# Optimization experiments

Measured on AMD Instinct MI355X. Metric: run time of the kernel, lower is better.

The kernel has to match this reference:

```python
import jax, jax.numpy as jnp
import numpy as np

D, H, B = 16, 1024, 2048  # input_size, hidden_size, batch
EPS = 1e-12


def _masks():
    # MADE degree assignment, order 'A' (natural order)
    deg_in = jnp.arange(1, D + 1)                # [D]
    deg_h = jnp.arange(H) % (D - 1) + 1          # [H]
    m0 = (deg_h[:, None] >= deg_in[None, :]).astype(jnp.float32)  # [H, D] input->hidden
    m1 = (deg_h[:, None] >= deg_h[None, :]).astype(jnp.float32)   # [H, H] hidden->hidden
    m2 = (deg_in[:, None] > deg_h[None, :]).astype(jnp.float32)   # [D, H] hidden->output
    return m0, m1, m2


def setup_inputs() -> dict:
    key = jax.random.key(0)
    ks = jax.random.split(key, 8)

    def lin(k, out_d, in_d):
        k1, k2, k3 = jax.random.split(k, 3)
        v = jax.random.normal(k1, (out_d, in_d), jnp.float32)
        g = jax.random.uniform(k2, (out_d,), jnp.float32, 0.1, 0.2)  # small gain keeps logstd stable over D iters
        b = jax.random.normal(k3, (out_d,), jnp.float32) * 0.01
        return v, g, b

    inp = {"x": jax.random.normal(ks[0], (B, D), jnp.float32)}
    dims = [(H, D), (H, H), (D, H)]
    i = 1
    for n in ("mu", "lv"):
        for j, (o, ii) in enumerate(dims):
            v, g, b = lin(ks[i], o, ii)
            i += 1
            inp[f"{n}_v{j}"] = v
            inp[f"{n}_g{j}"] = g
            inp[f"{n}_b{j}"] = b
    return inp


def _wn(v, g, m):
    # weight-normalized masked linear weight: mask * g * v / ||v||
    return m * (g[:, None] * v / jnp.linalg.norm(v, axis=1, keepdims=True))


def _made(y, p):
    (w0, b0), (w1, b1), (w2, b2) = p
    h = jax.nn.elu(y @ w0.T + b0)   # [B, H]
    h = jax.nn.elu(h @ w1.T + b1)   # [B, H]
    return h @ w2.T + b2            # [B, D]


def reference(x, mu_v0, mu_g0, mu_b0, mu_v1, mu_g1, mu_b1, mu_v2, mu_g2, mu_b2,
              lv_v0, lv_g0, lv_b0, lv_v1, lv_g1, lv_b1, lv_v2, lv_g2, lv_b2):
    m0, m1, m2 = _masks()
    pm = ((_wn(mu_v0, mu_g0, m0), mu_b0), (_wn(mu_v1, mu_g1, m1), mu_b1), (_wn(mu_v2, mu_g2, m2), mu_b2))
    pl = ((_wn(lv_v0, lv_g0, m0), lv_b0), (_wn(lv_v1, lv_g1, m1), lv_b1), (_wn(lv_v2, lv_g2, m2), lv_b2))

    def step(carry, _):
        y, _ls = carry
        mu = _made(y, pm)
        logstd = _made(y, pl) * 0.5
        y_new = (x - mu) / (jnp.exp(logstd) + EPS)
        return (y_new, logstd), None

    init = (jnp.zeros_like(x), jnp.zeros_like(x))
    (y, logstd), _ = jax.lax.scan(step, init, None, length=D)
    return y, logstd.sum(axis=1)
```

## Files before the change

kernel.cpp:

```cpp
#include <hip/hip_runtime.h>
#include <cstdint>
#include <cstddef>


#define Dd 16
#define Hh 1024
#define Bb 2048
#define EPSV 1e-12f

typedef unsigned short u16;
typedef __attribute__((ext_vector_type(4))) float f32x4;
typedef __attribute__((ext_vector_type(8))) short s16x8;
typedef __attribute__((ext_vector_type(4))) u16 u16x4;
typedef __attribute__((ext_vector_type(8))) u16 u16x8;

__device__ __forceinline__ u16 f2bf(float f) {
  union { float f; unsigned u; } v; v.f = f;
  unsigned u = v.u;
  unsigned r = (u + 0x7fffu + ((u >> 16) & 1u)) >> 16;
  return (u16)r;
}
__device__ __forceinline__ float elu(float a) {
  return a > 0.f ? a : __expf(a) - 1.f;
}
__device__ __forceinline__ void barrier_lds() {
  asm volatile("s_waitcnt lgkmcnt(0)" ::: "memory");
  __builtin_amdgcn_s_barrier();
}

__device__ __forceinline__ int p_of(int i) {
  if (i < 276) { int g = i / 69, q = i - g * 69; return g + 15 * q; }
  int r = i - 276; int g = 4 + r / 68, q = r - (g - 4) * 68;
  return g + 15 * q;
}
__device__ __forceinline__ int g_of(int i) {
  return (i < 276) ? (i / 69) : (4 + (i - 276) / 68);
}
__device__ __forceinline__ int lb_of(int g) {
  return (g <= 4) ? 69 * g : 276 + 68 * (g - 4);
}
__device__ __forceinline__ int sz_of(int g) { return (g < 4) ? 69 : 68; }

#define W2F_NET (15 * 3 * 512)
#define W0F_NET (15 * 5 * 512)

__global__ __launch_bounds__(256) void prep_all(
    const float* __restrict__ mu_v0, const float* __restrict__ mu_g0,
    const float* __restrict__ mu_b0,
    const float* __restrict__ mu_v1, const float* __restrict__ mu_g1,
    const float* __restrict__ mu_b1,
    const float* __restrict__ mu_v2, const float* __restrict__ mu_g2,
    const float* __restrict__ lv_v0, const float* __restrict__ lv_g0,
    const float* __restrict__ lv_b0,
    const float* __restrict__ lv_v1, const float* __restrict__ lv_g1,
    const float* __restrict__ lv_b1,
    const float* __restrict__ lv_v2, const float* __restrict__ lv_g2,
    u16* __restrict__ W1f, u16* __restrict__ W2f, u16* __restrict__ W0f,
    float* __restrict__ b1p, float* __restrict__ b0p) {
  int bid = blockIdx.x, tid = threadIdx.x;
  int l = tid & 63, w = tid >> 6;

  {
    int wid = bid * 4 + w;
    int net = wid / 1200, rem = wid % 1200;
    int g = rem / 80, u = rem % 80;
    u16* dstb = W1f + ((size_t)((net * 15 + g) * 16) * 10) * 512;
    const int nf = u >> 4, lane16 = u & 15;
    if (u < sz_of(g)) {
      int j = p_of(lb_of(g) + u);
      const float* v = (net ? lv_v1 : mu_v1) + (size_t)j * Hh;
      float val[4][4]; float ss = 0.f;
      for (int ii = 0; ii < 4; ++ii)
        for (int t = 0; t < 4; ++t) {
          int kp = ii * 256 + 4 * l + t;
          float xx = v[p_of(kp)];
          val[ii][t] = xx; ss += xx * xx;
        }
      for (int s = 32; s; s >>= 1) ss += __shfl_xor(ss, s);
      float sc = ((net ? lv_g1 : mu_g1)[j]) * rsqrtf(ss);
      for (int ii = 0; ii < 4; ++ii) {
        int k0 = ii * 256 + 4 * l;
        u16x4 wv;
        for (int t = 0; t < 4; ++t)
          wv[t] = f2bf((g >= g_of(k0 + t)) ? sc * val[ii][t] : 0.f);
        int kt = k0 >> 6, kk = (k0 >> 5) & 1;
        int lanep = lane16 + 16 * ((k0 & 31) >> 3);
        *(u16x4*)(dstb + (size_t)(kt * 10 + nf * 2 + kk) * 512 +
                  lanep * 8 + (k0 & 7)) = wv;
      }
      if (l == 0) b1p[wid] = (net ? lv_b1 : mu_b1)[j];
    } else {
      u16x4 z = {0, 0, 0, 0};
      for (int ii = 0; ii < 4; ++ii) {
        int k0 = ii * 256 + 4 * l;
        int kt = k0 >> 6, kk = (k0 >> 5) & 1;
        int lanep = lane16 + 16 * ((k0 & 31) >> 3);
        *(u16x4*)(dstb + (size_t)(kt * 10 + nf * 2 + kk) * 512 +
                  lanep * 8 + (k0 & 7)) = z;
      }
      if (l == 0) b1p[wid] = 0.f;
    }
  }

  if (bid < 8) {
    int wid2 = bid * 4 + w;
    int nn = wid2 >> 4, oi = wid2 & 15;
    const float* v = (nn ? lv_v2 : mu_v2) + (size_t)oi * Hh;
    float ss = 0.f;
    for (int ii = 0; ii < 4; ++ii) {
      f32x4 vv = *(const f32x4*)(v + ii * 256 + 4 * l);
      ss += vv[0]*vv[0] + vv[1]*vv[1] + vv[2]*vv[2] + vv[3]*vv[3];
    }
    for (int s = 32; s; s >>= 1) ss += __shfl_xor(ss, s);
    float sc = ((nn ? lv_g2 : mu_g2)[oi]) * rsqrtf(ss);
    for (int e = l; e < 180; e += 64) {
      int g = e / 12, r12 = e - g * 12;
      int c = r12 >> 2, lk2 = r12 & 3;
      u16x8 wv;
      for (int t = 0; t < 8; ++t) {
        int u = c * 32 + lk2 * 8 + t;
        float val = (u < sz_of(g) && oi > g) ? sc * v[p_of(lb_of(g) + u)]
                                             : 0.f;
        wv[t] = f2bf(val);
      }
      *(u16x8*)(W2f + (size_t)(nn * W2F_NET) + ((g * 3 + c) * 64 +
                (oi + 16 * lk2)) * 8) = wv;
    }
  }

  if (bid >= 8 && bid < 18) {
    int idx = (bid - 8) * 256 + tid;
    if (idx < 2400) {
      int nn = idx / 1200, rem = idx % 1200;
      int g = rem / 80, u = rem % 80;
      const int nf = u >> 4, lr16 = u & 15;
      float row[16];
      float bias = 0.f;
      if (u < sz_of(g)) {
        int j = p_of(lb_of(g) + u);
        const float* v = (nn ? lv_v0 : mu_v0) + j * Dd;
        float vv[16]; float ss = 0.f;
        for (int k = 0; k < 16; ++k) { vv[k] = v[k]; ss += vv[k] * vv[k]; }
        float sc = ((nn ? lv_g0 : mu_g0)[j]) * rsqrtf(ss);
        for (int k = 0; k < 16; ++k) row[k] = (g >= k) ? sc * vv[k] : 0.f;
        bias = (nn ? lv_b0 : mu_b0)[j];
      } else {
        for (int k = 0; k < 16; ++k) row[k] = 0.f;
      }
      for (int lk2 = 0; lk2 < 4; ++lk2) {
        u16x8 wv;
        for (int t = 0; t < 8; ++t) {
          int k = lk2 * 8 + t;
          wv[t] = f2bf((k < 16) ? row[k] : 0.f);
        }
        *(u16x8*)(W0f + (size_t)(nn * W0F_NET) + ((g * 5 + nf) * 64 +
                  (lr16 + 16 * lk2)) * 8) = wv;
      }
      b0p[nn * 1200 + g * 80 + u] = bias;
    }
  }
}

#define LOADF(DST, BASE, KT)                                                \
  {                                                                         \
    const u16* fp_ = (BASE) + (size_t)(KT) * 5120;                          \
    _Pragma("unroll") for (int nf_ = 0; nf_ < 5; ++nf_)                     \
      _Pragma("unroll") for (int kk_ = 0; kk_ < 2; ++kk_)                   \
        DST[nf_][kk_] = *(const s16x8*)(fp_ + (nf_ * 2 + kk_) * 512);       \
  }
#define MFMAI(SLOT, KT)                                                     \
  {                                                                         \
    s16x8 a0_ = *(const s16x8*)(&h0L[net][lr][(KT) * 64 + lk * 8]);         \
    s16x8 a1_ = *(const s16x8*)(&h0L[net][lr][(KT) * 64 + 32 + lk * 8]);    \
    _Pragma("unroll") for (int nf_ = 0; nf_ < 5; ++nf_) {                   \
      hacc[nf_] = __builtin_amdgcn_mfma_f32_16x16x32_bf16(                  \
          a0_, SLOT[nf_][0], hacc[nf_], 0, 0, 0);                           \
      hacc[nf_] = __builtin_amdgcn_mfma_f32_16x16x32_bf16(                  \
          a1_, SLOT[nf_][1], hacc[nf_], 0, 0, 0);                           \
    }                                                                       \
  }

__global__ __launch_bounds__(512, 1) void afmade_main(
    const u16* __restrict__ W1f, const u16* __restrict__ W2f,
    const u16* __restrict__ W0f,
    const float* __restrict__ b1p, const float* __restrict__ b0p,
    const float* __restrict__ b2_mu, const float* __restrict__ b2_lv,
    const float* __restrict__ x, float* __restrict__ out) {
  __shared__ u16 h0L[2][16][1040];
  __shared__ float sPart[2][4][16][80];
  __shared__ u16 sH1[2][16][104];
  __shared__ u16 yb[16][40];
  __shared__ float sX[16][16];
  __shared__ float sB1L[2400];
  __shared__ float sB0L[2400];
  __shared__ float sB2[2][16];
  __shared__ float sLsum[16];

  const int tid = threadIdx.x;
  const int l = tid & 63, w = tid >> 6;
  const int net = w >> 2, kq = w & 3;
  const int lr = l & 15, lk = l >> 4;
  const int b0g = blockIdx.x * 16;

  {
    u16x8 z = {0, 0, 0, 0, 0, 0, 0, 0};
    for (int e = tid; e < 4160; e += 512) ((u16x8*)h0L)[e] = z;
    for (int e = tid; e < 416; e += 512) ((u16x8*)sH1)[e] = z;
    for (int e = tid; e < 80; e += 512) ((u16x8*)yb)[e] = z;
  }
  for (int e = tid; e < 256; e += 512)
    sX[e >> 4][e & 15] = x[(size_t)(b0g + (e >> 4)) * 16 + (e & 15)];
  for (int e = tid; e < 2400; e += 512) { sB1L[e] = b1p[e]; sB0L[e] = b0p[e]; }
  if (tid < 16) sB2[0][tid] = b2_mu[tid];
  else if (tid < 32) sB2[1][tid - 16] = b2_lv[tid - 16];
  else if (tid < 48) sLsum[tid - 32] = 0.f;
  f32x4 mlacc0 = {0.f, 0.f, 0.f, 0.f};
  f32x4 mlacc1 = {0.f, 0.f, 0.f, 0.f};

  s16x8 bfA[5][2], bfB[5][2];
  {
    const u16* base1 = W1f + ((size_t)((net * 15 + 0) * 16) * 10) * 512 +
                       (size_t)l * 8;
    if (kq < 2) LOADF(bfA, base1, kq);
  }
  __syncthreads();

  for (int s = 0; s < 16; ++s) {
    s16x8 w0pre0, w0pre1;
    if (s < 15) {
      const u16* W0g = W0f + net * W0F_NET + s * (5 * 512);
      w0pre0 = *(const s16x8*)(W0g + (size_t)kq * 512 + l * 8);
      if (kq == 0)
        w0pre1 = *(const s16x8*)(W0g + (size_t)4 * 512 + l * 8);
    }

    if (s > 0) {
      const int g = s - 1;
      const int ktn = (lb_of(s) + 63) >> 6;
      const int ktnN = (s < 15) ? ((lb_of(s + 1) + 63) >> 6) : 0;
      const u16* baseg = W1f + ((size_t)((net * 15 + g) * 16) * 10) * 512 +
                         (size_t)l * 8;
      const u16* basen = W1f + ((size_t)((net * 15 + s) * 16) * 10) * 512 +
                         (size_t)l * 8;
      s16x8 w2f[6];
#pragma unroll
      for (int c = 0; c < 3; ++c) {
        w2f[c] = *(const s16x8*)(W2f + ((size_t)(g * 3 + c) * 64 + l) * 8);
        w2f[3 + c] = *(const s16x8*)(W2f + (size_t)W2F_NET +
                                     ((size_t)(g * 3 + c) * 64 + l) * 8);
      }
      f32x4 hacc[5] = {};
      if (kq + 4 < ktn)  LOADF(bfB, baseg, kq + 4);
      if (kq < ktn)      MFMAI(bfA, kq);
      if (kq + 8 < ktn)  LOADF(bfA, baseg, kq + 8);
      if (kq + 4 < ktn)  MFMAI(bfB, kq + 4);
      if (kq + 12 < ktn) LOADF(bfB, baseg, kq + 12);
      if (kq + 8 < ktn)  MFMAI(bfA, kq + 8);
      if (kq + 12 < ktn) MFMAI(bfB, kq + 12);
#pragma unroll
      for (int nf = 0; nf < 5; ++nf)
#pragma unroll
        for (int reg = 0; reg < 4; ++reg)
          sPart[net][kq][lk * 4 + reg][nf * 16 + lr] = hacc[nf][reg];
      if (s < 15 && kq < ktnN) LOADF(bfA, basen, kq);
      barrier_lds();
      {
        const int nn = tid >> 8;
        const int rr = (tid >> 4) & 15;
        const int u0 = tid & 15;
#pragma unroll
        for (int c = 0; c < 5; ++c) {
          int uu = c * 16 + u0;
          float v = sPart[nn][0][rr][uu] + sPart[nn][1][rr][uu] +
                    sPart[nn][2][rr][uu] + sPart[nn][3][rr][uu] +
                    sB1L[nn * 1200 + g * 80 + uu];
          sH1[nn][rr][uu] = f2bf(elu(v));
        }
      }
      barrier_lds();
#pragma unroll
      for (int c = 0; c < 3; ++c) {
        s16x8 a0 = *(const s16x8*)(&sH1[0][lr][c * 32 + lk * 8]);
        mlacc0 = __builtin_amdgcn_mfma_f32_16x16x32_bf16(
            a0, w2f[c], mlacc0, 0, 0, 0);
        s16x8 a1v = *(const s16x8*)(&sH1[1][lr][c * 32 + lk * 8]);
        mlacc1 = __builtin_amdgcn_mfma_f32_16x16x32_bf16(
            a1v, w2f[3 + c], mlacc1, 0, 0, 0);
      }
    }
    if (lr == s) {
#pragma unroll
      for (int reg = 0; reg < 4; ++reg) {
        int r = lk * 4 + reg;
        float mu = mlacc0[reg] + sB2[0][s];
        float lv = mlacc1[reg] + sB2[1][s];
        float ls = 0.5f * lv;
        float yv = (sX[r][s] - mu) / (__expf(ls) + EPSV);
        yb[r][s] = f2bf(yv);
        if (w == 0) {
          out[(size_t)(b0g + r) * 16 + s] = yv;
          float ns = sLsum[r] + ls;
          sLsum[r] = ns;
          if (s == 15) out[Bb * 16 + b0g + r] = ns;
        }
      }
    }
    asm volatile("s_waitcnt lgkmcnt(0)" ::: "memory");
    if (s < 15) {
      const int LbS = lb_of(s), szS = sz_of(s);
      s16x8 yfrag = *(const s16x8*)(&yb[lr][lk * 8]);
      {
        int unit = kq * 16 + lr;
        f32x4 h = __builtin_amdgcn_mfma_f32_16x16x32_bf16(
            yfrag, w0pre0, (f32x4){0.f, 0.f, 0.f, 0.f}, 0, 0, 0);
        if (unit < szS) {
          float bias = sB0L[net * 1200 + s * 80 + unit];
#pragma unroll
          for (int reg = 0; reg < 4; ++reg)
            h0L[net][lk * 4 + reg][LbS + unit] = f2bf(elu(h[reg] + bias));
        }
      }
      if (kq == 0) {
        int unit = 64 + lr;
        f32x4 h = __builtin_amdgcn_mfma_f32_16x16x32_bf16(
            yfrag, w0pre1, (f32x4){0.f, 0.f, 0.f, 0.f}, 0, 0, 0);
        if (unit < szS) {
          float bias = sB0L[net * 1200 + s * 80 + unit];
#pragma unroll
          for (int reg = 0; reg < 4; ++reg)
            h0L[net][lk * 4 + reg][LbS + unit] = f2bf(elu(h[reg] + bias));
        }
      }
      barrier_lds();
    }
  }
}


extern "C" void kernel_launch(void* const* d_in, const int* in_sizes, int n_in,
                              void* d_out, int out_size, void* d_ws, size_t ws_size,
                              hipStream_t stream) {
  const float* x     = (const float*)d_in[0];
  const float* mu_v0 = (const float*)d_in[1];
  const float* mu_g0 = (const float*)d_in[2];
  const float* mu_b0 = (const float*)d_in[3];
  const float* mu_v1 = (const float*)d_in[4];
  const float* mu_g1 = (const float*)d_in[5];
  const float* mu_b1 = (const float*)d_in[6];
  const float* mu_v2 = (const float*)d_in[7];
  const float* mu_g2 = (const float*)d_in[8];
  const float* mu_b2 = (const float*)d_in[9];
  const float* lv_v0 = (const float*)d_in[10];
  const float* lv_g0 = (const float*)d_in[11];
  const float* lv_b0 = (const float*)d_in[12];
  const float* lv_v1 = (const float*)d_in[13];
  const float* lv_g1 = (const float*)d_in[14];
  const float* lv_b1 = (const float*)d_in[15];
  const float* lv_v2 = (const float*)d_in[16];
  const float* lv_g2 = (const float*)d_in[17];
  const float* lv_b2 = (const float*)d_in[18];

  char* ws = (char*)d_ws;
  u16*   W1f = (u16*)(ws);
  u16*   W2f = (u16*)(ws + 4915200);
  u16*   W0f = (u16*)(ws + 5007360);
  float* b1p = (float*)(ws + 5160960);
  float* b0p = (float*)(ws + 5170560);

  prep_all<<<600, 256, 0, stream>>>(
      mu_v0, mu_g0, mu_b0, mu_v1, mu_g1, mu_b1, mu_v2, mu_g2,
      lv_v0, lv_g0, lv_b0, lv_v1, lv_g1, lv_b1, lv_v2, lv_g2,
      W1f, W2f, W0f, b1p, b0p);

  afmade_main<<<128, 512, 0, stream>>>(W1f, W2f, W0f, b1p, b0p,
                                       mu_b2, lv_b2, x, (float*)d_out);
}
```

Before: 70.59 us.

## Halve batch rows per block to launch 256 blocks with two blocks per CU

Each block now processes 8 batch rows instead of 16, doubling the grid to 256 blocks so more of the device's CUs are busy. Launch bounds allow two blocks per CU and LDS arrays shrink to fit. MFMA tiles stay 16-wide, so half of each MFMA's rows duplicate data (lr&7) and are masked out, which wastes matrix throughput and doubles total weight streaming from L2 per row.

```diff
diff --git a/kernel.cpp b/kernel.cpp
--- a/kernel.cpp
+++ b/kernel.cpp
@@ -170,8 +170,8 @@
   }
 #define MFMAI(SLOT, KT)                                                     \
   {                                                                         \
-    s16x8 a0_ = *(const s16x8*)(&h0L[net][lr][(KT) * 64 + lk * 8]);         \
-    s16x8 a1_ = *(const s16x8*)(&h0L[net][lr][(KT) * 64 + 32 + lk * 8]);    \
+    s16x8 a0_ = *(const s16x8*)(&h0L[net][lr & 7][(KT) * 64 + lk * 8]);     \
+    s16x8 a1_ = *(const s16x8*)(&h0L[net][lr & 7][(KT) * 64 + 32 + lk * 8]);\
     _Pragma("unroll") for (int nf_ = 0; nf_ < 5; ++nf_) {                   \
       hacc[nf_] = __builtin_amdgcn_mfma_f32_16x16x32_bf16(                  \
           a0_, SLOT[nf_][0], hacc[nf_], 0, 0, 0);                           \
@@ -180,40 +180,40 @@
     }                                                                       \
   }
 
-__global__ __launch_bounds__(512, 1) void afmade_main(
+__global__ __launch_bounds__(512, 2) void afmade_main(
     const u16* __restrict__ W1f, const u16* __restrict__ W2f,
     const u16* __restrict__ W0f,
     const float* __restrict__ b1p, const float* __restrict__ b0p,
     const float* __restrict__ b2_mu, const float* __restrict__ b2_lv,
     const float* __restrict__ x, float* __restrict__ out) {
-  __shared__ u16 h0L[2][16][1040];
-  __shared__ float sPart[2][4][16][80];
-  __shared__ u16 sH1[2][16][104];
-  __shared__ u16 yb[16][40];
-  __shared__ float sX[16][16];
+  __shared__ u16 h0L[2][8][1032];
+  __shared__ float sPart[2][4][8][84];
+  __shared__ u16 sH1[2][8][104];
+  __shared__ u16 yb[8][40];
+  __shared__ float sX[8][16];
   __shared__ float sB1L[2400];
   __shared__ float sB0L[2400];
   __shared__ float sB2[2][16];
-  __shared__ float sLsum[16];
+  __shared__ float sLsum[8];
 
   const int tid = threadIdx.x;
   const int l = tid & 63, w = tid >> 6;
   const int net = w >> 2, kq = w & 3;
   const int lr = l & 15, lk = l >> 4;
-  const int b0g = blockIdx.x * 16;
+  const int b0g = blockIdx.x * 8;
 
   {
     u16x8 z = {0, 0, 0, 0, 0, 0, 0, 0};
-    for (int e = tid; e < 4160; e += 512) ((u16x8*)h0L)[e] = z;
-    for (int e = tid; e < 416; e += 512) ((u16x8*)sH1)[e] = z;
-    for (int e = tid; e < 80; e += 512) ((u16x8*)yb)[e] = z;
-  }
-  for (int e = tid; e < 256; e += 512)
-    sX[e >> 4][e & 15] = x[(size_t)(b0g + (e >> 4)) * 16 + (e & 15)];
+    for (int e = tid; e < 2064; e += 512) ((u16x8*)h0L)[e] = z;
+    for (int e = tid; e < 208; e += 512) ((u16x8*)sH1)[e] = z;
+    if (tid < 40) ((u16x8*)yb)[tid] = z;
+  }
+  if (tid < 128)
+    sX[tid >> 4][tid & 15] = x[(size_t)(b0g + (tid >> 4)) * 16 + (tid & 15)];
   for (int e = tid; e < 2400; e += 512) { sB1L[e] = b1p[e]; sB0L[e] = b0p[e]; }
   if (tid < 16) sB2[0][tid] = b2_mu[tid];
   else if (tid < 32) sB2[1][tid - 16] = b2_lv[tid - 16];
-  else if (tid < 48) sLsum[tid - 32] = 0.f;
+  else if (tid < 40) sLsum[tid - 32] = 0.f;
   f32x4 mlacc0 = {0.f, 0.f, 0.f, 0.f};
   f32x4 mlacc1 = {0.f, 0.f, 0.f, 0.f};
 
@@ -260,30 +260,34 @@
 #pragma unroll
       for (int nf = 0; nf < 5; ++nf)
 #pragma unroll
-        for (int reg = 0; reg < 4; ++reg)
-          sPart[net][kq][lk * 4 + reg][nf * 16 + lr] = hacc[nf][reg];
+        for (int reg = 0; reg < 4; ++reg) {
+          int row = lk * 4 + reg;
+          if (row < 8) sPart[net][kq][row][nf * 16 + lr] = hacc[nf][reg];
+        }
       if (s < 15 && kq < ktnN) LOADF(bfA, basen, kq);
       barrier_lds();
       {
         const int nn = tid >> 8;
         const int rr = (tid >> 4) & 15;
         const int u0 = tid & 15;
-#pragma unroll
-        for (int c = 0; c < 5; ++c) {
-          int uu = c * 16 + u0;
-          float v = sPart[nn][0][rr][uu] + sPart[nn][1][rr][uu] +
-                    sPart[nn][2][rr][uu] + sPart[nn][3][rr][uu] +
-                    sB1L[nn * 1200 + g * 80 + uu];
-          sH1[nn][rr][uu] = f2bf(elu(v));
+        if (rr < 8) {
+#pragma unroll
+          for (int c = 0; c < 5; ++c) {
+            int uu = c * 16 + u0;
+            float v = sPart[nn][0][rr][uu] + sPart[nn][1][rr][uu] +
+                      sPart[nn][2][rr][uu] + sPart[nn][3][rr][uu] +
+                      sB1L[nn * 1200 + g * 80 + uu];
+            sH1[nn][rr][uu] = f2bf(elu(v));
+          }
         }
       }
       barrier_lds();
 #pragma unroll
       for (int c = 0; c < 3; ++c) {
-        s16x8 a0 = *(const s16x8*)(&sH1[0][lr][c * 32 + lk * 8]);
+        s16x8 a0 = *(const s16x8*)(&sH1[0][lr & 7][c * 32 + lk * 8]);
         mlacc0 = __builtin_amdgcn_mfma_f32_16x16x32_bf16(
             a0, w2f[c], mlacc0, 0, 0, 0);
-        s16x8 a1v = *(const s16x8*)(&sH1[1][lr][c * 32 + lk * 8]);
+        s16x8 a1v = *(const s16x8*)(&sH1[1][lr & 7][c * 32 + lk * 8]);
         mlacc1 = __builtin_amdgcn_mfma_f32_16x16x32_bf16(
             a1v, w2f[3 + c], mlacc1, 0, 0, 0);
       }
@@ -292,23 +296,25 @@
 #pragma unroll
       for (int reg = 0; reg < 4; ++reg) {
         int r = lk * 4 + reg;
-        float mu = mlacc0[reg] + sB2[0][s];
-        float lv = mlacc1[reg] + sB2[1][s];
-        float ls = 0.5f * lv;
-        float yv = (sX[r][s] - mu) / (__expf(ls) + EPSV);
-        yb[r][s] = f2bf(yv);
-        if (w == 0) {
-          out[(size_t)(b0g + r) * 16 + s] = yv;
-          float ns = sLsum[r] + ls;
-          sLsum[r] = ns;
-          if (s == 15) out[Bb * 16 + b0g + r] = ns;
+        if (r < 8) {
+          float mu = mlacc0[reg] + sB2[0][s];
+          float lv = mlacc1[reg] + sB2[1][s];
+          float ls = 0.5f * lv;
+          float yv = (sX[r][s] - mu) / (__expf(ls) + EPSV);
+          yb[r][s] = f2bf(yv);
+          if (w == 0) {
+            out[(size_t)(b0g + r) * 16 + s] = yv;
+            float ns = sLsum[r] + ls;
+            sLsum[r] = ns;
+            if (s == 15) out[Bb * 16 + b0g + r] = ns;
+          }
         }
       }
     }
     asm volatile("s_waitcnt lgkmcnt(0)" ::: "memory");
     if (s < 15) {
       const int LbS = lb_of(s), szS = sz_of(s);
-      s16x8 yfrag = *(const s16x8*)(&yb[lr][lk * 8]);
+      s16x8 yfrag = *(const s16x8*)(&yb[lr & 7][lk * 8]);
       {
         int unit = kq * 16 + lr;
         f32x4 h = __builtin_amdgcn_mfma_f32_16x16x32_bf16(
@@ -316,8 +322,11 @@
         if (unit < szS) {
           float bias = sB0L[net * 1200 + s * 80 + unit];
 #pragma unroll
-          for (int reg = 0; reg < 4; ++reg)
-            h0L[net][lk * 4 + reg][LbS + unit] = f2bf(elu(h[reg] + bias));
+          for (int reg = 0; reg < 4; ++reg) {
+            int row = lk * 4 + reg;
+            if (row < 8)
+              h0L[net][row][LbS + unit] = f2bf(elu(h[reg] + bias));
+          }
         }
       }
       if (kq == 0) {
@@ -327,8 +336,11 @@
         if (unit < szS) {
           float bias = sB0L[net * 1200 + s * 80 + unit];
 #pragma unroll
-          for (int reg = 0; reg < 4; ++reg)
-            h0L[net][lk * 4 + reg][LbS + unit] = f2bf(elu(h[reg] + bias));
+          for (int reg = 0; reg < 4; ++reg) {
+            int row = lk * 4 + reg;
+            if (row < 8)
+              h0L[net][row][LbS + unit] = f2bf(elu(h[reg] + bias));
+          }
         }
       }
       barrier_lds();
@@ -372,6 +384,6 @@
       lv_v0, lv_g0, lv_b0, lv_v1, lv_g1, lv_b1, lv_v2, lv_g2,
       W1f, W2f, W0f, b1p, b0p);
 
-  afmade_main<<<128, 512, 0, stream>>>(W1f, W2f, W0f, b1p, b0p,
+  afmade_main<<<256, 512, 0, stream>>>(W1f, W2f, W0f, b1p, b0p,
                                        mu_b2, lv_b2, x, (float*)d_out);
 }
```

After: 75.11 us. +6.4%, slower.

## Split hidden-layer GEMM across waves by output columns instead of K, drop partial-sum reduction

Applied to the files above, without the earlier changes.

Each wave now owns a slice of hidden output units (16 columns, with wave 0 also taking the extra 16) and runs the full K loop, instead of splitting K across four waves. This removes the sPart LDS partial-sum buffer, one barrier and the cross-wave reduction pass. Weight fragments are prefetched through a 4-slot ring of registers, and even/odd accumulators break the MFMA dependency chain. In exchange wave 0 carries twice the MFMA work, so the waves are unevenly loaded, and each wave does a longer serial K chain.

```diff
diff --git a/kernel.cpp b/kernel.cpp
--- a/kernel.cpp
+++ b/kernel.cpp
@@ -161,23 +161,46 @@
   }
 }
 
-#define LOADF(DST, BASE, KT)                                                \
+#define LDW(SLOT, KT, BASE)                                                 \
   {                                                                         \
-    const u16* fp_ = (BASE) + (size_t)(KT) * 5120;                          \
-    _Pragma("unroll") for (int nf_ = 0; nf_ < 5; ++nf_)                     \
-      _Pragma("unroll") for (int kk_ = 0; kk_ < 2; ++kk_)                   \
-        DST[nf_][kk_] = *(const s16x8*)(fp_ + (nf_ * 2 + kk_) * 512);       \
-  }
-#define MFMAI(SLOT, KT)                                                     \
-  {                                                                         \
+    const u16* p1_ = (BASE) + (size_t)((KT) * 10 + kq * 2) * 512 + l * 8;   \
+    f1[SLOT][0] = *(const s16x8*)(p1_);                                     \
+    f1[SLOT][1] = *(const s16x8*)(p1_ + 512);                               \
+    if (kq == 0) {                                                          \
+      const u16* p2_ = (BASE) + (size_t)((KT) * 10 + 8) * 512 + l * 8;      \
+      f2[SLOT][0] = *(const s16x8*)(p2_);                                   \
+      f2[SLOT][1] = *(const s16x8*)(p2_ + 512);                             \
+    }                                                                       \
+  }
+#define POS(KT)                                                             \
+  if ((KT) < ktn) {                                                         \
     s16x8 a0_ = *(const s16x8*)(&h0L[net][lr][(KT) * 64 + lk * 8]);         \
     s16x8 a1_ = *(const s16x8*)(&h0L[net][lr][(KT) * 64 + 32 + lk * 8]);    \
-    _Pragma("unroll") for (int nf_ = 0; nf_ < 5; ++nf_) {                   \
-      hacc[nf_] = __builtin_amdgcn_mfma_f32_16x16x32_bf16(                  \
-          a0_, SLOT[nf_][0], hacc[nf_], 0, 0, 0);                           \
-      hacc[nf_] = __builtin_amdgcn_mfma_f32_16x16x32_bf16(                  \
-          a1_, SLOT[nf_][1], hacc[nf_], 0, 0, 0);                           \
+    if ((KT) & 1) {                                                         \
+      acc1O = __builtin_amdgcn_mfma_f32_16x16x32_bf16(                      \
+          a0_, f1[(KT) & 3][0], acc1O, 0, 0, 0);                            \
+      acc1O = __builtin_amdgcn_mfma_f32_16x16x32_bf16(                      \
+          a1_, f1[(KT) & 3][1], acc1O, 0, 0, 0);                            \
+    } else {                                                                \
+      acc1E = __builtin_amdgcn_mfma_f32_16x16x32_bf16(                      \
+          a0_, f1[(KT) & 3][0], acc1E, 0, 0, 0);                            \
+      acc1E = __builtin_amdgcn_mfma_f32_16x16x32_bf16(                      \
+          a1_, f1[(KT) & 3][1], acc1E, 0, 0, 0);                            \
     }                                                                       \
+    if (kq == 0) {                                                          \
+      if ((KT) & 1) {                                                       \
+        acc2O = __builtin_amdgcn_mfma_f32_16x16x32_bf16(                    \
+            a0_, f2[(KT) & 3][0], acc2O, 0, 0, 0);                          \
+        acc2O = __builtin_amdgcn_mfma_f32_16x16x32_bf16(                    \
+            a1_, f2[(KT) & 3][1], acc2O, 0, 0, 0);                          \
+      } else {                                                              \
+        acc2E = __builtin_amdgcn_mfma_f32_16x16x32_bf16(                    \
+            a0_, f2[(KT) & 3][0], acc2E, 0, 0, 0);                          \
+        acc2E = __builtin_amdgcn_mfma_f32_16x16x32_bf16(                    \
+            a1_, f2[(KT) & 3][1], acc2E, 0, 0, 0);                          \
+      }                                                                     \
+    }                                                                       \
+    if ((KT) + 4 < ktn) LDW((KT) & 3, (KT) + 4, baseg);                     \
   }
 
 __global__ __launch_bounds__(512, 1) void afmade_main(
@@ -187,7 +210,6 @@
     const float* __restrict__ b2_mu, const float* __restrict__ b2_lv,
     const float* __restrict__ x, float* __restrict__ out) {
   __shared__ u16 h0L[2][16][1040];
-  __shared__ float sPart[2][4][16][80];
   __shared__ u16 sH1[2][16][104];
   __shared__ u16 yb[16][40];
   __shared__ float sX[16][16];
@@ -217,11 +239,12 @@
   f32x4 mlacc0 = {0.f, 0.f, 0.f, 0.f};
   f32x4 mlacc1 = {0.f, 0.f, 0.f, 0.f};
 
-  s16x8 bfA[5][2], bfB[5][2];
+  s16x8 f1[4][2], f2[4][2];
   {
-    const u16* base1 = W1f + ((size_t)((net * 15 + 0) * 16) * 10) * 512 +
+    const u16* base0 = W1f + ((size_t)((net * 15 + 0) * 16) * 10) * 512 +
                        (size_t)l * 8;
-    if (kq < 2) LOADF(bfA, base1, kq);
+    LDW(0, 0, base0);
+    LDW(1, 1, base0);
   }
   __syncthreads();
 
@@ -249,33 +272,31 @@
         w2f[3 + c] = *(const s16x8*)(W2f + (size_t)W2F_NET +
                                      ((size_t)(g * 3 + c) * 64 + l) * 8);
       }
-      f32x4 hacc[5] = {};
-      if (kq + 4 < ktn)  LOADF(bfB, baseg, kq + 4);
-      if (kq < ktn)      MFMAI(bfA, kq);
-      if (kq + 8 < ktn)  LOADF(bfA, baseg, kq + 8);
-      if (kq + 4 < ktn)  MFMAI(bfB, kq + 4);
-      if (kq + 12 < ktn) LOADF(bfB, baseg, kq + 12);
-      if (kq + 8 < ktn)  MFMAI(bfA, kq + 8);
-      if (kq + 12 < ktn) MFMAI(bfB, kq + 12);
-#pragma unroll
-      for (int nf = 0; nf < 5; ++nf)
+      f32x4 acc1E = {0.f, 0.f, 0.f, 0.f}, acc1O = {0.f, 0.f, 0.f, 0.f};
+      f32x4 acc2E = {0.f, 0.f, 0.f, 0.f}, acc2O = {0.f, 0.f, 0.f, 0.f};
+      POS(0)  POS(1)  POS(2)  POS(3)  POS(4)  POS(5)  POS(6)  POS(7)
+      POS(8)  POS(9)  POS(10) POS(11) POS(12) POS(13) POS(14) POS(15)
+      {
+        int unit = kq * 16 + lr;
+        float b1v = sB1L[net * 1200 + g * 80 + unit];
+        f32x4 s1 = acc1E + acc1O;
 #pragma unroll
         for (int reg = 0; reg < 4; ++reg)
-          sPart[net][kq][lk * 4 + reg][nf * 16 + lr] = hacc[nf][reg];
-      if (s < 15 && kq < ktnN) LOADF(bfA, basen, kq);
-      barrier_lds();
-      {
-        const int nn = tid >> 8;
-        const int rr = (tid >> 4) & 15;
-        const int u0 = tid & 15;
-#pragma unroll
-        for (int c = 0; c < 5; ++c) {
-          int uu = c * 16 + u0;
-          float v = sPart[nn][0][rr][uu] + sPart[nn][1][rr][uu] +
-                    sPart[nn][2][rr][uu] + sPart[nn][3][rr][uu] +
-                    sB1L[nn * 1200 + g * 80 + uu];
-          sH1[nn][rr][uu] = f2bf(elu(v));
-        }
+          sH1[net][lk * 4 + reg][unit] = f2bf(elu(s1[reg] + b1v));
+        if (kq == 0) {
+          int unit2 = 64 + lr;
+          float b2v = sB1L[net * 1200 + g * 80 + unit2];
+          f32x4 s2 = acc2E + acc2O;
+#pragma unroll
+          for (int reg = 0; reg < 4; ++reg)
+            sH1[net][lk * 4 + reg][unit2] = f2bf(elu(s2[reg] + b2v));
+        }
+      }
+      if (s < 15) {
+        LDW(0, 0, basen);
+        LDW(1, 1, basen);
+        if (2 < ktnN) LDW(2, 2, basen);
+        if (3 < ktnN) LDW(3, 3, basen);
       }
       barrier_lds();
 #pragma unroll
```

Measured after the change: 81.85 us. +15.9%, slower.
